# Kernel tuning notes

Measured on AMD Instinct MI355X. Metric: run time of the kernel, lower is better.

Reference implementation:

```python
import jax, jax.numpy as jnp
import numpy as np

N_NODES = 50000


def _gcn_conv(x, W, b, src, dst, norm, n_nodes):
    # x: [N, Fin], W: [Fin, Fout]
    h = x @ W                                   # [N, Fout]
    msg = h[src] * norm[:, None]                # [E+N, Fout] edge messages
    out = jax.ops.segment_sum(msg, dst, num_segments=n_nodes)
    return out + b


def reference(x, edge_index, W1, b1, W2, b2):
    n = x.shape[0]
    # add self-loops (PyG GCNConv default add_self_loops=True)
    loop = jnp.arange(n, dtype=edge_index.dtype)
    src = jnp.concatenate([edge_index[0], loop])
    dst = jnp.concatenate([edge_index[1], loop])
    # symmetric degree normalization: deg over destination with unit weights
    deg = jax.ops.segment_sum(jnp.ones_like(dst, dtype=x.dtype), dst, num_segments=n)
    dinv = jnp.where(deg > 0, jax.lax.rsqrt(deg), 0.0)
    norm = dinv[src] * dinv[dst]                # [E+N]
    h = _gcn_conv(x, W1, b1, src, dst, norm, n)
    h = jax.nn.relu(h)
    out = _gcn_conv(h, W2, b2, src, dst, norm, n)
    return out


def setup_inputs() -> dict:
    key = jax.random.key(0)
    k1, k2, k3, k4 = jax.random.split(key, 4)
    n, e, fin, hid, fout = N_NODES, 800000, 128, 128, 64
    x = jax.random.normal(k1, (n, fin), dtype=jnp.float32)
    edge_index = jax.random.randint(k2, (2, e), 0, n, dtype=jnp.int64)
    # Glorot-ish init for linear weights, zero bias (PyG default)
    W1 = jax.random.normal(k3, (fin, hid), dtype=jnp.float32) / np.sqrt(fin)
    b1 = jnp.zeros((hid,), dtype=jnp.float32)
    W2 = jax.random.normal(k4, (hid, fout), dtype=jnp.float32) / np.sqrt(hid)
    b2 = jnp.zeros((fout,), dtype=jnp.float32)
    return {"x": x, "edge_index": edge_index, "W1": W1, "b1": b1, "W2": W2, "b2": b2}
```

## Files before the change

kernel.cpp:

```cpp
#include <hip/hip_runtime.h>
#include <hip/hip_bf16.h>


constexpr int FIN = 128;
constexpr int HID = 128;
constexpr int FOUT = 64;
constexpr int CAP = 48;
constexpr int NPB = 98;
constexpr int BCAP = 3072;
constexpr int OVF_MAX = 65536;

typedef __attribute__((ext_vector_type(8))) short s16x8;
typedef __attribute__((ext_vector_type(4))) float f32x4;

static __device__ __forceinline__ float bf2f(__hip_bfloat16 v) { return __bfloat162float(v); }
static __device__ __forceinline__ float lo2f(unsigned u) { union { unsigned i; float f; } c; c.i = u << 16; return c.f; }
static __device__ __forceinline__ float hi2f(unsigned u) { union { unsigned i; float f; } c; c.i = u & 0xffff0000u; return c.f; }
static __device__ __forceinline__ unsigned short f2bfu(float f) {
    __hip_bfloat16 h = __float2bfloat16(f);
    union { __hip_bfloat16 h; unsigned short u; } c; c.h = h; return c.u;
}
static __device__ __forceinline__ unsigned pack2(float a, float b) {
    return (unsigned)f2bfu(a) | ((unsigned)f2bfu(b) << 16);
}
static __device__ __forceinline__ void acc_add(float* acc, uint4 v) {
    acc[0] += lo2f(v.x); acc[1] += hi2f(v.x);
    acc[2] += lo2f(v.y); acc[3] += hi2f(v.y);
    acc[4] += lo2f(v.z); acc[5] += hi2f(v.z);
    acc[6] += lo2f(v.w); acc[7] += hi2f(v.w);
}

__global__ __launch_bounds__(256) void k_detect(const unsigned* __restrict__ xw,
                                                const int* __restrict__ eiw,
                                                int E, int* __restrict__ flags,
                                                int* __restrict__ gcur) {
    for (int i = threadIdx.x; i < 1026; i += 256) gcur[i] = 0;
    __shared__ int s_bf16like, s_oddnz;
    if (threadIdx.x == 0) { s_bf16like = 0; s_oddnz = 0; }
    __syncthreads();
    int c = 0;
    for (int i = threadIdx.x; i < 4096; i += 256) {
        unsigned ex = ((xw[i] & 0xffffu) >> 7) & 0xffu;
        if (ex >= 117u && ex <= 130u) c++;
    }
    atomicAdd(&s_bf16like, c);
    int nz = 0;
    for (int i = threadIdx.x; i < 2048; i += 256)
        if (eiw[2 * i + 1] != 0) nz++;
    atomicAdd(&s_oddnz, nz);
    __syncthreads();
    if (threadIdx.x == 0) {
        flags[0] = (s_bf16like < 2048) ? 1 : 0;
        flags[1] = (s_oddnz == 0) ? 1 : 0;
    }
}

__global__ __launch_bounds__(256) void k_binA(const int* __restrict__ ei, int E, int N,
                                              int nbuk,
                                              int* __restrict__ gcur,
                                              int2* __restrict__ pairs,
                                              int2* __restrict__ ovfA,
                                              int* __restrict__ ovfAcnt,
                                              const int* __restrict__ flags) {
    __shared__ int hist[1024];
    __shared__ int gbase[1024];
    const int tid = threadIdx.x;
    const long base = (long)blockIdx.x * 4096;
    const bool i64 = flags[1] != 0;
    for (int b = tid; b < nbuk; b += 256) hist[b] = 0;
    __syncthreads();
    for (int j = 0; j < 16; ++j) {
        long i = base + j * 256 + tid;
        if (i >= E) break;
        int s, d;
        if (i64) { s = ((const int2*)ei)[i].x; d = ((const int2*)(ei + 2 * (long)E))[i].x; }
        else     { s = ei[i]; d = ei[(long)E + i]; }
        if ((unsigned)s >= (unsigned)N || (unsigned)d >= (unsigned)N) continue;
        atomicAdd(&hist[d / NPB], 1);
    }
    __syncthreads();
    for (int b = tid; b < nbuk; b += 256) {
        int h = hist[b];
        gbase[b] = h > 0 ? atomicAdd(&gcur[b], h) : 0;
        hist[b] = 0;
    }
    __syncthreads();
    for (int j = 0; j < 16; ++j) {
        long i = base + j * 256 + tid;
        if (i >= E) break;
        int s, d;
        if (i64) { s = ((const int2*)ei)[i].x; d = ((const int2*)(ei + 2 * (long)E))[i].x; }
        else     { s = ei[i]; d = ei[(long)E + i]; }
        if ((unsigned)s >= (unsigned)N || (unsigned)d >= (unsigned)N) continue;
        int b = d / NPB;
        int p = gbase[b] + atomicAdd(&hist[b], 1);
        if (p < BCAP) {
            pairs[(long)b * BCAP + p] = make_int2(d, s);
        } else {
            int op = atomicAdd(ovfAcnt, 1);
            if (op < OVF_MAX) ovfA[op] = make_int2(d, s);
        }
    }
}

__global__ __launch_bounds__(256) void k_binB(const int* __restrict__ gcur,
                                              const int2* __restrict__ pairs,
                                              int* __restrict__ cnt,
                                              int* __restrict__ slots,
                                              int2* __restrict__ ovf2,
                                              int* __restrict__ ovf2cnt, int N) {
    __shared__ int cntL[NPB];
    __shared__ __align__(16) int slotsL[NPB * CAP];
    const int b = blockIdx.x;
    const int tid = threadIdx.x;
    const int d0 = b * NPB;
    const int nd = min(NPB, N - d0);
    if (nd <= 0) return;
    for (int i = tid; i < NPB; i += 256) cntL[i] = 0;
    __syncthreads();
    const int c = min(gcur[b], BCAP);
    const int2* pb = pairs + (long)b * BCAP;
    for (int i = tid; i < c; i += 256) {
        int2 p = pb[i];
        int ld = p.x - d0;
        int pos = atomicAdd(&cntL[ld], 1);
        if (pos < CAP) {
            slotsL[ld * CAP + pos] = p.y;
        } else {
            int op = atomicAdd(ovf2cnt, 1);
            if (op < OVF_MAX) ovf2[op] = p;
        }
    }
    __syncthreads();
    for (int i = tid; i < nd; i += 256) cnt[d0 + i] = cntL[i];
    const uint4* sv = (const uint4*)slotsL;
    uint4* gv = (uint4*)(slots + (long)d0 * CAP);
    const int total4 = (nd * CAP) >> 2;
    for (int i = tid; i < total4; i += 256) gv[i] = sv[i];
}

__global__ __launch_bounds__(256) void k_patch(const int2* __restrict__ ovfA,
                                               const int* __restrict__ ovfAcnt,
                                               int* __restrict__ cnt,
                                               int* __restrict__ slots,
                                               int2* __restrict__ ovf2,
                                               int* __restrict__ ovf2cnt, int N) {
    int n = *ovfAcnt; n = n < OVF_MAX ? n : OVF_MAX;
    for (int i = blockIdx.x * 256 + threadIdx.x; i < n; i += gridDim.x * 256) {
        int2 p = ovfA[i];
        int pos = atomicAdd(&cnt[p.x], 1);
        if (pos < CAP) {
            slots[(long)p.x * CAP + pos] = p.y;
        } else {
            int op = atomicAdd(ovf2cnt, 1);
            if (op < OVF_MAX) ovf2[op] = p;
        }
    }
}

template<int CT>
__global__ __launch_bounds__(256) void k_gemm(const void* __restrict__ Xp, int x_follows_flag,
                                              const void* __restrict__ Wp,
                                              const int* __restrict__ cnt,
                                              __hip_bfloat16* __restrict__ G,
                                              const int* __restrict__ flags, int N) {
    constexpr int C = CT * 16;
    __shared__ __align__(16) short Wt[C * 136];
    const bool f32m = flags[0] != 0;
    const bool xf32 = (x_follows_flag != 0) && f32m;
    const int tid = threadIdx.x;
    for (int i = tid; i < 128 * C; i += 256) {
        int k = i / C, n = i % C;
        float wv = f32m ? ((const float*)Wp)[(long)k * C + n]
                        : bf2f(((const __hip_bfloat16*)Wp)[(long)k * C + n]);
        Wt[n * 136 + k] = (short)f2bfu(wv);
    }
    __syncthreads();
    const int w = tid >> 6, lane = tid & 63;
    const int m = lane & 15, quad = lane >> 4;
    const int rowA = blockIdx.x * 64 + w * 16 + m;
    const int rowc = rowA < N ? rowA : N - 1;
    s16x8 afr[4];
#pragma unroll
    for (int kc = 0; kc < 4; ++kc) {
        const int k0 = kc * 32 + quad * 8;
        if (!xf32) {
            afr[kc] = *(const s16x8*)((const __hip_bfloat16*)Xp + (long)rowc * 128 + k0);
        } else {
            const float* p = (const float*)Xp + (long)rowc * 128 + k0;
            s16x8 t;
#pragma unroll
            for (int j = 0; j < 8; ++j) t[j] = (short)f2bfu(p[j]);
            afr[kc] = t;
        }
    }
    const int rbase = blockIdx.x * 64 + w * 16 + quad * 4;
    float dv[4];
#pragma unroll
    for (int r = 0; r < 4; ++r) {
        int rr = min(rbase + r, N - 1);
        dv[r] = rsqrtf((float)(cnt[rr] + 1));
    }
#pragma unroll
    for (int ct = 0; ct < CT; ++ct) {
        f32x4 acc = {0.f, 0.f, 0.f, 0.f};
#pragma unroll
        for (int kc = 0; kc < 4; ++kc) {
            s16x8 bfr = *(const s16x8*)&Wt[(ct * 16 + m) * 136 + kc * 32 + quad * 8];
            acc = __builtin_amdgcn_mfma_f32_16x16x32_bf16(afr[kc], bfr, acc, 0, 0, 0);
        }
#pragma unroll
        for (int r = 0; r < 4; ++r) {
            int rr = rbase + r;
            if (rr < N) G[(long)rr * C + ct * 16 + m] = __float2bfloat16(dv[r] * acc[r]);
        }
    }
}

template<int F, int LAYER1>
__global__ __launch_bounds__(256) void k_gather(const __hip_bfloat16* __restrict__ G,
                                                const int* __restrict__ cnt,
                                                const int* __restrict__ slots,
                                                const int2* __restrict__ ovf2,
                                                const int* __restrict__ ovf2cnt,
                                                const void* __restrict__ bias,
                                                void* __restrict__ outp,
                                                const int* __restrict__ flags, int N) {
    constexpr int L = F / 8;
    constexpr int NODES = 256 / L;
    const int tid = threadIdx.x;
    const int grp = tid / L, lane = tid % L;
    const int node = blockIdx.x * NODES + grp;
    if (node >= N) return;
    const int cd = cnt[node];
    const float wself = rsqrtf((float)(cd + 1));
    const int m = cd < CAP ? cd : CAP;
    const int* sl = slots + (long)node * CAP;
    float acc[8] = {0, 0, 0, 0, 0, 0, 0, 0};
    acc_add(acc, ((const uint4*)(G + (long)node * F))[lane]);
    int i = 0;
    for (; i + 3 < m; i += 4) {
        int s0 = sl[i], s1 = sl[i + 1], s2 = sl[i + 2], s3 = sl[i + 3];
        uint4 v0 = ((const uint4*)(G + (long)s0 * F))[lane];
        uint4 v1 = ((const uint4*)(G + (long)s1 * F))[lane];
        uint4 v2 = ((const uint4*)(G + (long)s2 * F))[lane];
        uint4 v3 = ((const uint4*)(G + (long)s3 * F))[lane];
        acc_add(acc, v0); acc_add(acc, v1); acc_add(acc, v2); acc_add(acc, v3);
    }
    for (; i < m; ++i)
        acc_add(acc, ((const uint4*)(G + (long)sl[i] * F))[lane]);
    if (cd > CAP) {
        int oc = *ovf2cnt; oc = oc < OVF_MAX ? oc : OVF_MAX;
        for (int j = 0; j < oc; ++j)
            if (ovf2[j].x == node)
                acc_add(acc, ((const uint4*)(G + (long)ovf2[j].y * F))[lane]);
    }
    const bool f32m = flags[0] != 0;
    const int c0 = lane * 8;
    float bv[8];
    if (f32m) {
        const float4* bp = (const float4*)((const float*)bias + c0);
        float4 b0 = bp[0], b1 = bp[1];
        bv[0] = b0.x; bv[1] = b0.y; bv[2] = b0.z; bv[3] = b0.w;
        bv[4] = b1.x; bv[5] = b1.y; bv[6] = b1.z; bv[7] = b1.w;
    } else {
        uint4 b = *(const uint4*)((const __hip_bfloat16*)bias + c0);
        bv[0] = lo2f(b.x); bv[1] = hi2f(b.x); bv[2] = lo2f(b.y); bv[3] = hi2f(b.y);
        bv[4] = lo2f(b.z); bv[5] = hi2f(b.z); bv[6] = lo2f(b.w); bv[7] = hi2f(b.w);
    }
    float o[8];
#pragma unroll
    for (int c = 0; c < 8; ++c) {
        float v = wself * acc[c] + bv[c];
        o[c] = (LAYER1 && v < 0.f) ? 0.f : v;
    }
    if (LAYER1 || !f32m) {
        uint4 pv = { pack2(o[0], o[1]), pack2(o[2], o[3]), pack2(o[4], o[5]), pack2(o[6], o[7]) };
        ((uint4*)outp)[(long)node * L + lane] = pv;
    } else {
        float4* op = (float4*)((float*)outp + (long)node * F + c0);
        op[0] = make_float4(o[0], o[1], o[2], o[3]);
        op[1] = make_float4(o[4], o[5], o[6], o[7]);
    }
}

extern "C" void kernel_launch(void* const* d_in, const int* in_sizes, int n_in,
                              void* d_out, int out_size, void* d_ws, size_t ws_size,
                              hipStream_t stream) {
    const void* x  = d_in[0];
    const int*  ei = (const int*)d_in[1];
    const void* W1 = d_in[2];
    const void* b1 = d_in[3];
    const void* W2 = d_in[4];
    const void* b2 = d_in[5];

    const int N = in_sizes[0] / FIN;
    const int E = in_sizes[1] / 2;
    const int nbuk = (N + NPB - 1) / NPB;

    char* ws = (char*)d_ws;
    int*   flags   = (int*)ws;
    int*   gcur    = (int*)(ws + 4096);
    int*   ovfAcnt = gcur + 1024;
    int*   ovf2cnt = gcur + 1025;
    int*   cnt     = (int*)(ws + 65536);
    int2*  ovfA    = (int2*)(ws + 524288);
    int2*  ovf2    = (int2*)(ws + 1048576);
    int*   slots   = (int*)(ws + 2097152);
    __hip_bfloat16* g  = (__hip_bfloat16*)(ws + 11730944);
    __hip_bfloat16* g2 = g;
    int2*  pairs   = (int2*)(ws + 24530944);
    __hip_bfloat16* h1 = (__hip_bfloat16*)(ws + 24530944);

    const int GB = (N + 63) / 64;
    const int AB = (E + 4095) / 4096;

    k_detect<<<1, 256, 0, stream>>>((const unsigned*)x, ei, E, flags, gcur);
    k_binA<<<AB, 256, 0, stream>>>(ei, E, N, nbuk, gcur, pairs, ovfA, ovfAcnt, flags);
    k_binB<<<nbuk, 256, 0, stream>>>(gcur, pairs, cnt, slots, ovf2, ovf2cnt, N);
    k_patch<<<32, 256, 0, stream>>>(ovfA, ovfAcnt, cnt, slots, ovf2, ovf2cnt, N);
    k_gemm<8><<<GB, 256, 0, stream>>>(x, 1, W1, cnt, g, flags, N);
    k_gather<128, 1><<<(N + 15) / 16, 256, 0, stream>>>(g, cnt, slots, ovf2, ovf2cnt, b1, h1, flags, N);
    k_gemm<4><<<GB, 256, 0, stream>>>(h1, 0, W2, cnt, g2, flags, N);
    k_gather<64, 0><<<(N + 31) / 32, 256, 0, stream>>>(g2, cnt, slots, ovf2, ovf2cnt, b2, d_out, flags, N);
}
```

Before: 204.7 us.

## Split gather into column tiles and cache edges in registers in binning

The gather kernels now split the feature dimension into 32-column tiles. Each block processes 64 nodes for one tile, and the low bits of the block index interleave tiles and node sub-groups. The aim is to shrink the per-pass working set of gathered rows so more of it stays in cache, at the cost of rereading each node's slot list once per tile. The binning kernel now uses smaller blocks and keeps the loaded edge endpoints in registers between the histogram pass and the scatter pass, so the edge list is not read twice. Its shared histogram shrinks to 512 buckets, which relies on the bucket count staying at or below that.

```diff
diff --git a/kernel.cpp b/kernel.cpp
--- a/kernel.cpp
+++ b/kernel.cpp
@@ -34,7 +34,7 @@
                                                 const int* __restrict__ eiw,
                                                 int E, int* __restrict__ flags,
                                                 int* __restrict__ gcur) {
-    for (int i = threadIdx.x; i < 1026; i += 256) gcur[i] = 0;
+    for (int i = threadIdx.x; i < 514; i += 256) gcur[i] = 0;
     __shared__ int s_bf16like, s_oddnz;
     if (threadIdx.x == 0) { s_bf16like = 0; s_oddnz = 0; }
     __syncthreads();
@@ -62,21 +62,25 @@
                                               int2* __restrict__ ovfA,
                                               int* __restrict__ ovfAcnt,
                                               const int* __restrict__ flags) {
-    __shared__ int hist[1024];
-    __shared__ int gbase[1024];
+    __shared__ int hist[512];
+    __shared__ int gbase[512];
     const int tid = threadIdx.x;
-    const long base = (long)blockIdx.x * 4096;
+    const long base = (long)blockIdx.x * 2048;
     const bool i64 = flags[1] != 0;
+    int se[8], de[8];
     for (int b = tid; b < nbuk; b += 256) hist[b] = 0;
     __syncthreads();
-    for (int j = 0; j < 16; ++j) {
+#pragma unroll
+    for (int j = 0; j < 8; ++j) {
         long i = base + j * 256 + tid;
-        if (i >= E) break;
-        int s, d;
-        if (i64) { s = ((const int2*)ei)[i].x; d = ((const int2*)(ei + 2 * (long)E))[i].x; }
-        else     { s = ei[i]; d = ei[(long)E + i]; }
-        if ((unsigned)s >= (unsigned)N || (unsigned)d >= (unsigned)N) continue;
-        atomicAdd(&hist[d / NPB], 1);
+        int s = 0, d = -1;
+        if (i < E) {
+            if (i64) { s = ((const int2*)ei)[i].x; d = ((const int2*)(ei + 2 * (long)E))[i].x; }
+            else     { s = ei[i]; d = ei[(long)E + i]; }
+            if ((unsigned)s >= (unsigned)N || (unsigned)d >= (unsigned)N) d = -1;
+        }
+        se[j] = s; de[j] = d;
+        if (d >= 0) atomicAdd(&hist[d / NPB], 1);
     }
     __syncthreads();
     for (int b = tid; b < nbuk; b += 256) {
@@ -85,20 +89,17 @@
         hist[b] = 0;
     }
     __syncthreads();
-    for (int j = 0; j < 16; ++j) {
-        long i = base + j * 256 + tid;
-        if (i >= E) break;
-        int s, d;
-        if (i64) { s = ((const int2*)ei)[i].x; d = ((const int2*)(ei + 2 * (long)E))[i].x; }
-        else     { s = ei[i]; d = ei[(long)E + i]; }
-        if ((unsigned)s >= (unsigned)N || (unsigned)d >= (unsigned)N) continue;
+#pragma unroll
+    for (int j = 0; j < 8; ++j) {
+        int d = de[j];
+        if (d < 0) continue;
         int b = d / NPB;
         int p = gbase[b] + atomicAdd(&hist[b], 1);
         if (p < BCAP) {
-            pairs[(long)b * BCAP + p] = make_int2(d, s);
+            pairs[(long)b * BCAP + p] = make_int2(d, se[j]);
         } else {
             int op = atomicAdd(ovfAcnt, 1);
-            if (op < OVF_MAX) ovfA[op] = make_int2(d, s);
+            if (op < OVF_MAX) ovfA[op] = make_int2(d, se[j]);
         }
     }
 }
@@ -217,7 +218,7 @@
     }
 }
 
-template<int F, int LAYER1>
+template<int F, int TILES, int LAYER1>
 __global__ __launch_bounds__(256) void k_gather(const __hip_bfloat16* __restrict__ G,
                                                 const int* __restrict__ cnt,
                                                 const int* __restrict__ slots,
@@ -226,37 +227,41 @@
                                                 const void* __restrict__ bias,
                                                 void* __restrict__ outp,
                                                 const int* __restrict__ flags, int N) {
-    constexpr int L = F / 8;
-    constexpr int NODES = 256 / L;
+    constexpr int SUBS = 8 / TILES;
+    const int h = blockIdx.x & 7;
+    const int nc = blockIdx.x >> 3;
+    const int tile = h / SUBS;
+    const int sub = h % SUBS;
     const int tid = threadIdx.x;
-    const int grp = tid / L, lane = tid % L;
-    const int node = blockIdx.x * NODES + grp;
+    const int grp = tid >> 2, lane = tid & 3;
+    const int node = nc * (64 * SUBS) + sub * 64 + grp;
     if (node >= N) return;
     const int cd = cnt[node];
     const float wself = rsqrtf((float)(cd + 1));
     const int m = cd < CAP ? cd : CAP;
     const int* sl = slots + (long)node * CAP;
+    const __hip_bfloat16* Gt = G + tile * 32;
     float acc[8] = {0, 0, 0, 0, 0, 0, 0, 0};
-    acc_add(acc, ((const uint4*)(G + (long)node * F))[lane]);
+    acc_add(acc, ((const uint4*)(Gt + (long)node * F))[lane]);
     int i = 0;
     for (; i + 3 < m; i += 4) {
         int s0 = sl[i], s1 = sl[i + 1], s2 = sl[i + 2], s3 = sl[i + 3];
-        uint4 v0 = ((const uint4*)(G + (long)s0 * F))[lane];
-        uint4 v1 = ((const uint4*)(G + (long)s1 * F))[lane];
-        uint4 v2 = ((const uint4*)(G + (long)s2 * F))[lane];
-        uint4 v3 = ((const uint4*)(G + (long)s3 * F))[lane];
+        uint4 v0 = ((const uint4*)(Gt + (long)s0 * F))[lane];
+        uint4 v1 = ((const uint4*)(Gt + (long)s1 * F))[lane];
+        uint4 v2 = ((const uint4*)(Gt + (long)s2 * F))[lane];
+        uint4 v3 = ((const uint4*)(Gt + (long)s3 * F))[lane];
         acc_add(acc, v0); acc_add(acc, v1); acc_add(acc, v2); acc_add(acc, v3);
     }
     for (; i < m; ++i)
-        acc_add(acc, ((const uint4*)(G + (long)sl[i] * F))[lane]);
+        acc_add(acc, ((const uint4*)(Gt + (long)sl[i] * F))[lane]);
     if (cd > CAP) {
         int oc = *ovf2cnt; oc = oc < OVF_MAX ? oc : OVF_MAX;
         for (int j = 0; j < oc; ++j)
             if (ovf2[j].x == node)
-                acc_add(acc, ((const uint4*)(G + (long)ovf2[j].y * F))[lane]);
+                acc_add(acc, ((const uint4*)(Gt + (long)ovf2[j].y * F))[lane]);
     }
     const bool f32m = flags[0] != 0;
-    const int c0 = lane * 8;
+    const int c0 = tile * 32 + lane * 8;
     float bv[8];
     if (f32m) {
         const float4* bp = (const float4*)((const float*)bias + c0);
@@ -276,7 +281,7 @@
     }
     if (LAYER1 || !f32m) {
         uint4 pv = { pack2(o[0], o[1]), pack2(o[2], o[3]), pack2(o[4], o[5]), pack2(o[6], o[7]) };
-        ((uint4*)outp)[(long)node * L + lane] = pv;
+        ((uint4*)outp)[(long)node * (F / 8) + tile * 4 + lane] = pv;
     } else {
         float4* op = (float4*)((float*)outp + (long)node * F + c0);
         op[0] = make_float4(o[0], o[1], o[2], o[3]);
@@ -301,8 +306,8 @@
     char* ws = (char*)d_ws;
     int*   flags   = (int*)ws;
     int*   gcur    = (int*)(ws + 4096);
-    int*   ovfAcnt = gcur + 1024;
-    int*   ovf2cnt = gcur + 1025;
+    int*   ovfAcnt = gcur + 512;
+    int*   ovf2cnt = gcur + 513;
     int*   cnt     = (int*)(ws + 65536);
     int2*  ovfA    = (int2*)(ws + 524288);
     int2*  ovf2    = (int2*)(ws + 1048576);
@@ -313,14 +318,14 @@
     __hip_bfloat16* h1 = (__hip_bfloat16*)(ws + 24530944);
 
     const int GB = (N + 63) / 64;
-    const int AB = (E + 4095) / 4096;
+    const int AB = (E + 2047) / 2048;
 
     k_detect<<<1, 256, 0, stream>>>((const unsigned*)x, ei, E, flags, gcur);
     k_binA<<<AB, 256, 0, stream>>>(ei, E, N, nbuk, gcur, pairs, ovfA, ovfAcnt, flags);
     k_binB<<<nbuk, 256, 0, stream>>>(gcur, pairs, cnt, slots, ovf2, ovf2cnt, N);
     k_patch<<<32, 256, 0, stream>>>(ovfA, ovfAcnt, cnt, slots, ovf2, ovf2cnt, N);
     k_gemm<8><<<GB, 256, 0, stream>>>(x, 1, W1, cnt, g, flags, N);
-    k_gather<128, 1><<<(N + 15) / 16, 256, 0, stream>>>(g, cnt, slots, ovf2, ovf2cnt, b1, h1, flags, N);
+    k_gather<128, 4, 1><<<((N + 127) / 128) * 8, 256, 0, stream>>>(g, cnt, slots, ovf2, ovf2cnt, b1, h1, flags, N);
     k_gemm<4><<<GB, 256, 0, stream>>>(h1, 0, W2, cnt, g2, flags, N);
-    k_gather<64, 0><<<(N + 31) / 32, 256, 0, stream>>>(g2, cnt, slots, ovf2, ovf2cnt, b2, d_out, flags, N);
-}
+    k_gather<64, 2, 0><<<((N + 255) / 256) * 8, 256, 0, stream>>>(g2, cnt, slots, ovf2, ovf2cnt, b2, d_out, flags, N);
+}
```

After: 233.9 us. 14.3% more time.
